# Performance work log

Measured on AMD Instinct MI355X. Metric: run time of the kernel, lower is better.

## Reference

```python
import jax, jax.numpy as jnp
from jax import lax
import numpy as np

DEPTH = 4
D_MODEL = 192
D_INNER = 384
D_STATE = 16
D_CONV = 4
DT_RANK = 12
STRIDE = 4
NUM_PATCHES = 400
L_SEQ = NUM_PATCHES + 1  # +1 cls token appended at the end
EPS = 1e-5


def _rmsnorm(x, w):
    x = x.astype(jnp.float32)
    return (x * lax.rsqrt(jnp.mean(x * x, axis=-1, keepdims=True) + EPS)) * w


def _mamba(x, in_w, cw, cb, xp_w, dtw, dtb, A_log, Dv, ow):
    # x: [B, L, D_MODEL]
    B = x.shape[0]
    xz = jnp.einsum('bld,ed->ble', x, in_w)            # [B, L, 2*D_INNER]
    u, z = jnp.split(xz, 2, axis=-1)                   # [B, L, D_INNER] each
    # causal depthwise conv over L
    u_t = jnp.transpose(u, (0, 2, 1))                  # [B, D_INNER, L]
    u_pad = jnp.pad(u_t, ((0, 0), (0, 0), (D_CONV - 1, 0)))
    conv = lax.conv_general_dilated(
        u_pad, cw[:, None, :], (1,), 'VALID',
        dimension_numbers=('NCH', 'OIH', 'NCH'),
        feature_group_count=D_INNER)                   # [B, D_INNER, L]
    u = jax.nn.silu(conv + cb[:, None])
    u = jnp.transpose(u, (0, 2, 1))                    # [B, L, D_INNER]
    xdbl = jnp.einsum('bld,ed->ble', u, xp_w)          # [B, L, 44]
    dt, Bm, Cm = jnp.split(xdbl, [DT_RANK, DT_RANK + D_STATE], axis=-1)
    dt = jax.nn.softplus(jnp.einsum('blr,dr->bld', dt, dtw) + dtb)  # [B, L, D_INNER]
    A = -jnp.exp(A_log)                                # [D_INNER, D_STATE]
    dA = jnp.exp(dt[..., None] * A)                    # [B, L, D_INNER, D_STATE]
    dBu = dt[..., None] * Bm[:, :, None, :] * u[..., None]
    h0 = jnp.zeros((B, D_INNER, D_STATE), dtype=dA.dtype)

    def step(h, inp):
        dA_t, dBu_t = inp
        h = dA_t * h + dBu_t
        return h, h

    _, hs = lax.scan(step, h0, (jnp.swapaxes(dA, 0, 1), jnp.swapaxes(dBu, 0, 1)))
    hs = jnp.swapaxes(hs, 0, 1)                        # [B, L, D_INNER, D_STATE]
    y = jnp.einsum('bldn,bln->bld', hs, Cm) + u * Dv
    y = y * jax.nn.silu(z)
    return jnp.einsum('bld,ed->ble', y, ow)            # [B, L, D_MODEL]


def _forward(imgs, patch_w, patch_b, pos_embed, cls_token, norm_w, in_proj_w,
             conv_w, conv_b, xproj_w, dt_w, dt_b, A_log, D_param, out_w,
             normf_w, head_w, head_b):
    B = imgs.shape[0]
    # StrideEmbed: non-overlapping strides of 4 bytes -> linear to embed_dim
    x = imgs.reshape(B, NUM_PATCHES, STRIDE) @ patch_w + patch_b  # [B, 400, 192]
    x = x + pos_embed[:, :-1, :]
    cls = cls_token + pos_embed[:, -1:, :]             # [1, 1, 192]
    x = jnp.concatenate([x, jnp.broadcast_to(cls, (B, 1, D_MODEL))], axis=1)
    hidden = x
    residual = None
    for i in range(DEPTH):
        residual = hidden if residual is None else hidden + residual  # fp32 residual stream
        h = _rmsnorm(residual, norm_w[i])
        hidden = _mamba(h, in_proj_w[i], conv_w[i], conv_b[i], xproj_w[i],
                        dt_w[i], dt_b[i], A_log[i], D_param[i], out_w[i])
    x = _rmsnorm(hidden + residual, normf_w)
    cls_out = x[:, -1, :]                              # [B, 192]
    logits = cls_out @ head_w.T + head_b               # [B, 1000]
    return logits


def setup_inputs() -> dict:
    key = jax.random.key(0)
    ks = jax.random.split(key, 16)
    B = 32
    rn = lambda k, s, sc: jax.random.normal(k, s, dtype=jnp.float32) * sc
    A_log = jnp.broadcast_to(jnp.log(jnp.arange(1.0, D_STATE + 1.0, dtype=jnp.float32)),
                             (DEPTH, D_INNER, D_STATE))
    return {
        'imgs': rn(ks[0], (B, 1, 40, 40), 1.0),
        'patch_w': rn(ks[1], (STRIDE, D_MODEL), 0.1),
        'patch_b': jnp.zeros((D_MODEL,), jnp.float32),
        'pos_embed': rn(ks[2], (1, L_SEQ, D_MODEL), 0.02),
        'cls_token': rn(ks[3], (1, 1, D_MODEL), 0.02),
        'norm_w': jnp.ones((DEPTH, D_MODEL), jnp.float32),
        'in_proj_w': rn(ks[4], (DEPTH, 2 * D_INNER, D_MODEL), 0.05),
        'conv_w': rn(ks[5], (DEPTH, D_INNER, D_CONV), 0.3),
        'conv_b': jnp.zeros((DEPTH, D_INNER), jnp.float32),
        'xproj_w': rn(ks[6], (DEPTH, DT_RANK + 2 * D_STATE, D_INNER), 0.05),
        'dt_w': rn(ks[7], (DEPTH, D_INNER, DT_RANK), 0.1),
        'dt_b': rn(ks[8], (DEPTH, D_INNER), 0.5) - 4.0,
        'A_log': A_log,
        'D_param': jnp.ones((DEPTH, D_INNER), jnp.float32),
        'out_w': rn(ks[9], (DEPTH, D_MODEL, D_INNER), 0.05),
        'normf_w': jnp.ones((D_MODEL,), jnp.float32),
        'head_w': rn(ks[10], (1000, D_MODEL), 0.05),
        'head_b': jnp.zeros((1000,), jnp.float32),
    }


def reference(imgs, patch_w, patch_b, pos_embed, cls_token, norm_w, in_proj_w,
              conv_w, conv_b, xproj_w, dt_w, dt_b, A_log, D_param, out_w,
              normf_w, head_w, head_b):
    return _forward(imgs, patch_w, patch_b, pos_embed, cls_token, norm_w,
                    in_proj_w, conv_w, conv_b, xproj_w, dt_w, dt_b, A_log,
                    D_param, out_w, normf_w, head_w, head_b)
```

## Files before the change

### kernel.cpp

```cpp
#include <hip/hip_runtime.h>
#include <hip/hip_bf16.h>

#define B_SZ 32
#define LSEQ 401
#define NT (B_SZ * LSEQ)
#define DM 192
#define DI 384
#define DS 16
#define EPSF 1e-5f
#define NCH 16

typedef __attribute__((ext_vector_type(8))) short short8;
typedef __attribute__((ext_vector_type(4))) float f32x4;
typedef __hip_bfloat16 bf16;

#define OFF_IMGS    0
#define OFF_PATCHW  51200
#define OFF_PATCHB  51968
#define OFF_POS     52160
#define OFF_CLS     129152
#define OFF_NORMW   129344
#define OFF_INW     130112
#define OFF_CONVW   719936
#define OFF_CONVB   726080
#define OFF_XPROJW  727616
#define OFF_DTW     795200
#define OFF_DTB     813632
#define OFF_ALOG    815168
#define OFF_DP      839744
#define OFF_OUTW    841280
#define OFF_NORMF   1136192
#define OFF_HEADW   1136384
#define OFF_HEADB   1328384
#define OFF_TOTAL   1329384

#define WB_INW   0
#define WB_XPJ   589824
#define WB_OUT   688128
#define WB_DTW   983040
#define WB_TOTAL 1032192

__device__ __forceinline__ int chunk_s(int c) { return c == 0 ? 0 : 25 * c + 1; }
__device__ __forceinline__ int chunk_e(int c) { return 25 * c + 26; }

__device__ __forceinline__ float ldsrc(const void* p, int off, int isbf) {
  return isbf ? __bfloat162float(((const bf16*)p)[off]) : ((const float*)p)[off];
}
__device__ __forceinline__ float fast_silu(float z) {
  return z * __builtin_amdgcn_rcpf(1.f + __expf(-z));
}
__device__ __forceinline__ float fast_softplus(float x) {
  float e = __expf(x);
  return (x > 15.f) ? x : __logf(1.f + e);
}
__device__ __forceinline__ float bfbits(unsigned short u) {
  return __uint_as_float(((unsigned int)u) << 16);
}

#define DPP_ADD(x, ctrl) \
  x += __int_as_float(__builtin_amdgcn_update_dpp(0, __float_as_int(x), ctrl, 0xF, 0xF, true))
__device__ __forceinline__ float row_sum16(float x) {
  DPP_ADD(x, 0xB1);
  DPP_ADD(x, 0x4E);
  DPP_ADD(x, 0x124);
  DPP_ADD(x, 0x128);
  return x;
}

struct P18 { const void* p[18]; };

__global__ __launch_bounds__(256) void k_convwb(P18 t, float* __restrict__ fin,
                                                bf16* __restrict__ wb) {
  static const int st[19] = {OFF_IMGS, OFF_PATCHW, OFF_PATCHB, OFF_POS, OFF_CLS,
                             OFF_NORMW, OFF_INW, OFF_CONVW, OFF_CONVB, OFF_XPROJW,
                             OFF_DTW, OFF_DTB, OFF_ALOG, OFF_DP, OFF_OUTW,
                             OFF_NORMF, OFF_HEADW, OFF_HEADB, OFF_TOTAL};
  int isbf = (((const unsigned short*)t.p[5])[0] == 0x3F80) ? 1 : 0;
  int idx = blockIdx.x * 256 + threadIdx.x;
  if (idx < OFF_TOTAL) {
    int lo = 0;
#pragma unroll
    for (int i = 1; i < 18; ++i) if (idx >= st[i]) lo = i;
    fin[idx] = ldsrc(t.p[lo], idx - st[lo], isbf);
  } else if (idx < OFF_TOTAL + WB_TOTAL) {
    int j = idx - OFF_TOTAL;
    float v;
    if (j < WB_XPJ) {
      v = ldsrc(t.p[6], j, isbf);
    } else if (j < WB_OUT) {
      int i2 = j - WB_XPJ;
      int l = i2 / (64 * 384);
      int r = (i2 / 384) & 63;
      int k = i2 % 384;
      v = (r < 44) ? ldsrc(t.p[9], l * 44 * 384 + r * 384 + k, isbf) : 0.f;
    } else if (j < WB_DTW) {
      v = ldsrc(t.p[14], j - WB_OUT, isbf);
    } else {
      int i2 = j - WB_DTW;
      int l = i2 / (384 * 32);
      int r = i2 % (384 * 32);
      int d = r >> 5;
      int k = r & 31;
      v = (k < 12) ? ldsrc(t.p[10], l * 4608 + d * 12 + k, isbf) : 0.f;
    }
    wb[j] = __float2bfloat16(v);
  }
}

__device__ __forceinline__ void inproj32(const bf16 (*shb)[200],
                                         const bf16* __restrict__ Win,
                                         bf16* __restrict__ xb,
                                         bf16* __restrict__ zb,
                                         int row0, int tid) {
  int lane = tid & 63, wave = tid >> 6;
  int q = lane >> 4, mlo = lane & 15;
  short8 afrA[6], afrB[6];
#pragma unroll
  for (int kk = 0; kk < 6; ++kk) {
    afrA[kk] = *(const short8*)&shb[mlo][kk * 32 + q * 8];
    afrB[kk] = *(const short8*)&shb[16 + mlo][kk * 32 + q * 8];
  }
  const bf16* wbase = Win + (size_t)(wave * 96 + mlo) * DM + q * 8;
#pragma unroll
  for (int jh = 0; jh < 2; ++jh) {
    short8 Bb[18];
#pragma unroll
    for (int j = 0; j < 3; ++j)
#pragma unroll
      for (int kk = 0; kk < 6; ++kk)
        Bb[j * 6 + kk] = *(const short8*)(wbase + (size_t)(jh * 3 + j) * 16 * DM + kk * 32);
#pragma unroll
    for (int j = 0; j < 3; ++j) {
      f32x4 aA = {}, aB = {};
#pragma unroll
      for (int kk = 0; kk < 6; ++kk) {
        aA = __builtin_amdgcn_mfma_f32_16x16x32_bf16(afrA[kk], Bb[j * 6 + kk], aA, 0, 0, 0);
        aB = __builtin_amdgcn_mfma_f32_16x16x32_bf16(afrB[kk], Bb[j * 6 + kk], aB, 0, 0, 0);
      }
      int n = wave * 96 + (jh * 3 + j) * 16 + mlo;
      if (n < DI) {
#pragma unroll
        for (int i = 0; i < 4; ++i) {
          xb[(size_t)(row0 + q * 4 + i) * DI + n] = __float2bfloat16(aA[i]);
          xb[(size_t)(row0 + 16 + q * 4 + i) * DI + n] = __float2bfloat16(aB[i]);
        }
      } else {
        int nz = n - DI;
#pragma unroll
        for (int i = 0; i < 4; ++i) {
          zb[(size_t)(row0 + q * 4 + i) * DI + nz] = __float2bfloat16(aA[i]);
          zb[(size_t)(row0 + 16 + q * 4 + i) * DI + nz] = __float2bfloat16(aB[i]);
        }
      }
    }
  }
}

__global__ __launch_bounds__(512)
__attribute__((amdgpu_waves_per_eu(2, 2)))
void k_embedin(const float* __restrict__ fin,
               float* __restrict__ residual,
               const bf16* __restrict__ Win,
               bf16* __restrict__ xb,
               bf16* __restrict__ zb) {
  __shared__ bf16 shb[32][200];
  const float* imgs = fin + OFF_IMGS;
  const float* pw   = fin + OFF_PATCHW;
  const float* pb   = fin + OFF_PATCHB;
  const float* pos  = fin + OFF_POS;
  const float* cls  = fin + OFF_CLS;
  const float* nw0  = fin + OFF_NORMW;
  int tid = threadIdx.x;
  int row0 = blockIdx.x * 32;
  {
    int row = tid >> 4, g = tid & 15;
    int t = row0 + row;
    int b = t / LSEQ, l = t % LSEQ;
    float im[4];
    if (l < 400) {
#pragma unroll
      for (int s = 0; s < 4; ++s) im[s] = imgs[b * 1600 + l * 4 + s];
    }
    float rn[12], ss = 0.f;
#pragma unroll
    for (int k = 0; k < 12; ++k) {
      int col = g + 16 * k;
      float v;
      if (l < 400) {
        v = pb[col] + pos[l * DM + col];
#pragma unroll
        for (int s = 0; s < 4; ++s) v = fmaf(im[s], pw[s * DM + col], v);
      } else {
        v = cls[col] + pos[400 * DM + col];
      }
      residual[(size_t)t * DM + col] = v;
      rn[k] = v;
      ss = fmaf(v, v, ss);
    }
    ss = row_sum16(ss);
    float sres = rsqrtf(ss / (float)DM + EPSF);
#pragma unroll
    for (int k = 0; k < 12; ++k) {
      int col = g + 16 * k;
      shb[row][col] = __float2bfloat16(rn[k] * sres * nw0[col]);
    }
  }
  __syncthreads();
  inproj32(shb, Win, xb, zb, row0, tid);
}

__global__ __launch_bounds__(512) void k_xdt(const bf16* __restrict__ xb,
                                             const float* __restrict__ cw,
                                             const float* __restrict__ cb,
                                             const bf16* __restrict__ Wbf,
                                             float* __restrict__ xdbl,
                                             const bf16* __restrict__ dtwb,
                                             const float* __restrict__ dtb,
                                             bf16* __restrict__ ub,
                                             bf16* __restrict__ dto) {
  __shared__ bf16  sxt[19][392];
  __shared__ bf16  su[16][392];
  __shared__ float4 scw4[384];
  __shared__ float scb[384];
  __shared__ float sxp[2][16][48];
  __shared__ bf16  sxb[16][32];
  int row0 = blockIdx.x * 16;
  int tid = threadIdx.x;
  for (int i = tid; i < 19 * 48; i += 512) {
    int r = i / 48, c8 = i - r * 48;
    int t = row0 - 3 + r;
    if (t < 0) t = 0;
    *(short8*)&sxt[r][c8 * 8] = *(const short8*)(xb + (size_t)t * DI + c8 * 8);
  }
  for (int i = tid; i < 384; i += 512) {
    scw4[i] = ((const float4*)cw)[i];
    scb[i] = cb[i];
  }
  __syncthreads();
  for (int i = tid; i < 768; i += 512) {
    int tok = i / 48;
    int c8 = i - tok * 48;
    int d0 = c8 * 8;
    int t = row0 + tok;
    int l = t % LSEQ;
    float xr[4][8];
#pragma unroll
    for (int k = 0; k < 4; ++k) {
      short8 v = *(const short8*)&sxt[tok + k][d0];
      bool ok = (l - 3 + k) >= 0;
#pragma unroll
      for (int j = 0; j < 8; ++j) {
        unsigned int uu = ((unsigned int)(unsigned short)v[j]) << 16;
        xr[k][j] = ok ? __uint_as_float(uu) : 0.f;
      }
    }
    short8 uvv;
#pragma unroll
    for (int j = 0; j < 8; ++j) {
      float4 w = scw4[d0 + j];
      float a = scb[d0 + j];
      a = fmaf(xr[0][j], w.x, a);
      a = fmaf(xr[1][j], w.y, a);
      a = fmaf(xr[2][j], w.z, a);
      a = fmaf(xr[3][j], w.w, a);
      bf16 h = __float2bfloat16(fast_silu(a));
      uvv[j] = *reinterpret_cast<short*>(&h);
    }
    *(short8*)&su[tok][d0] = uvv;
    *(short8*)(ub + (size_t)t * DI + d0) = uvv;
  }
  __syncthreads();
  int lane = tid & 63;
  int wave = tid >> 6;
  int q = lane >> 4;
  int mlo = lane & 15;
  if (wave < 6) {
    int colw = (wave % 3) * 16;
    int kh = wave / 3;
    f32x4 acc = {};
    for (int k0 = 0; k0 < 192; k0 += 32) {
      short8 a = *(const short8*)&su[mlo][kh * 192 + k0 + q * 8];
      short8 b = *(const short8*)(Wbf + (size_t)(colw + mlo) * DI + kh * 192 + k0 + q * 8);
      acc = __builtin_amdgcn_mfma_f32_16x16x32_bf16(a, b, acc, 0, 0, 0);
    }
#pragma unroll
    for (int i = 0; i < 4; ++i) sxp[kh][q * 4 + i][colw + mlo] = acc[i];
  }
  __syncthreads();
  for (int i = tid; i < 16 * 44; i += 512) {
    int r = i / 44, c = i - r * 44;
    xdbl[(size_t)(row0 + r) * 44 + c] = sxp[0][r][c] + sxp[1][r][c];
  }
  for (int i = tid; i < 512; i += 512) {
    int tok = i >> 5, k = i & 31;
    sxb[tok][k] = __float2bfloat16(k < 12 ? sxp[0][tok][k] + sxp[1][tok][k] : 0.f);
  }
  __syncthreads();
  short8 afrag = *(const short8*)&sxb[mlo][q * 8];
#pragma unroll
  for (int jt = 0; jt < 3; ++jt) {
    int d = (wave * 3 + jt) * 16 + mlo;
    short8 bfrag = *(const short8*)(dtwb + (size_t)d * 32 + q * 8);
    f32x4 acc = {};
    acc = __builtin_amdgcn_mfma_f32_16x16x32_bf16(afrag, bfrag, acc, 0, 0, 0);
    float dtbv = dtb[d];
#pragma unroll
    for (int i = 0; i < 4; ++i)
      dto[(size_t)(row0 + q * 4 + i) * DI + d] =
          __float2bfloat16(fast_softplus(acc[i] + dtbv));
  }
}

__global__ __launch_bounds__(384)
__attribute__((amdgpu_waves_per_eu(2, 2)))
void k_scanA(const bf16* __restrict__ ub,
             const bf16* __restrict__ dtv,
             const float* __restrict__ xdbl,
             const float* __restrict__ A_log,
             float* __restrict__ Sq,
             float* __restrict__ Hq) {
  __shared__ float sB[26][16];
  int cc = blockIdx.x, b = blockIdx.y;
  int d = threadIdx.x;
  int s = chunk_s(cc), tc = chunk_e(cc) - s;
  int base = b * LSEQ;
  for (int i = d; i < tc * 16; i += 384) {
    int t = i >> 4, col = i & 15;
    sB[t][col] = xdbl[(size_t)(base + s + t) * 44 + 12 + col];
  }
  __syncthreads();
  float A[16], h[16];
#pragma unroll
  for (int j = 0; j < 4; ++j) {
    f32x4 al = *(const f32x4*)&A_log[d * DS + j * 4];
#pragma unroll
    for (int i = 0; i < 4; ++i) { A[j * 4 + i] = -__expf(al[i]); h[j * 4 + i] = 0.f; }
  }
  float S = 0.f;
  const unsigned short* pd = (const unsigned short*)(dtv + (size_t)(base + s) * DI + d);
  const unsigned short* pu = (const unsigned short*)(ub  + (size_t)(base + s) * DI + d);
  unsigned short dN = *pd, uN = *pu;
  for (int t = 0; t < tc; ++t) {
    unsigned short dC = dN, uC = uN;
    if (t + 1 < tc) { pd += DI; pu += DI; dN = *pd; uN = *pu; }
    float dv = bfbits(dC), uv = bfbits(uC);
    float w = dv * uv;
    S += dv;
    f32x4 B0 = *(const f32x4*)&sB[t][0];
    f32x4 B1 = *(const f32x4*)&sB[t][4];
    f32x4 B2 = *(const f32x4*)&sB[t][8];
    f32x4 B3 = *(const f32x4*)&sB[t][12];
#pragma unroll
    for (int n = 0; n < 16; ++n) {
      float Bn = (n < 4) ? B0[n] : (n < 8) ? B1[n - 4] : (n < 12) ? B2[n - 8] : B3[n - 12];
      float E = __expf(dv * A[n]);
      h[n] = fmaf(E, h[n], w * Bn);
    }
  }
  size_t si = ((size_t)cc * B_SZ + b) * 384 + d;
  Sq[si] = S;
#pragma unroll
  for (int j = 0; j < 4; ++j) {
    f32x4 hv;
#pragma unroll
    for (int i = 0; i < 4; ++i) hv[i] = h[j * 4 + i];
    *(f32x4*)&Hq[si * 16 + j * 4] = hv;
  }
}

__global__ __launch_bounds__(256) void k_scanP(const float* __restrict__ A_log,
                                               const float* __restrict__ Sq,
                                               float* __restrict__ Hq) {
  int idx = blockIdx.x * 256 + threadIdx.x;
  int n = idx & 15;
  int dd = (idx >> 4) % 384;
  int b = idx / (384 * 16);
  float A = -__expf(A_log[dd * DS + n]);
  float hs = 0.f;
  for (int c = 0; c < NCH - 1; ++c) {
    size_t si = ((size_t)c * B_SZ + b) * 384 + dd;
    float P = __expf(A * Sq[si]);
    size_t hi = si * 16 + n;
    float he = Hq[hi];
    hs = fmaf(P, hs, he);
    Hq[hi] = hs;
  }
}

__global__ __launch_bounds__(384)
__attribute__((amdgpu_waves_per_eu(2, 2)))
void k_scanB(const bf16* __restrict__ zb,
             const bf16* __restrict__ ub,
             const bf16* __restrict__ dtv,
             const float* __restrict__ xdbl,
             const float* __restrict__ A_log,
             const float* __restrict__ Dp,
             const float* __restrict__ Hq,
             bf16* __restrict__ yb) {
  __shared__ float sB[26][16], sC[26][16];
  int cc = blockIdx.x, b = blockIdx.y;
  int d = threadIdx.x;
  int s = chunk_s(cc), tc = chunk_e(cc) - s;
  int base = b * LSEQ;
  for (int i = d; i < tc * 32; i += 384) {
    int t = i >> 5, col = i & 31;
    float v = xdbl[(size_t)(base + s + t) * 44 + 12 + col];
    if (col < 16) sB[t][col] = v;
    else          sC[t][col - 16] = v;
  }
  __syncthreads();
  float A[16], h[16];
#pragma unroll
  for (int j = 0; j < 4; ++j) {
    f32x4 al = *(const f32x4*)&A_log[d * DS + j * 4];
#pragma unroll
    for (int i = 0; i < 4; ++i) A[j * 4 + i] = -__expf(al[i]);
  }
  if (cc == 0) {
#pragma unroll
    for (int n = 0; n < 16; ++n) h[n] = 0.f;
  } else {
    size_t hi = (((size_t)(cc - 1) * B_SZ + b) * 384 + d) * 16;
#pragma unroll
    for (int j = 0; j < 4; ++j) {
      f32x4 hv = *(const f32x4*)&Hq[hi + j * 4];
#pragma unroll
      for (int i = 0; i < 4; ++i) h[j * 4 + i] = hv[i];
    }
  }
  float Dv = Dp[d];
  const unsigned short* pd = (const unsigned short*)(dtv + (size_t)(base + s) * DI + d);
  const unsigned short* pu = (const unsigned short*)(ub  + (size_t)(base + s) * DI + d);
  const unsigned short* pz = (const unsigned short*)(zb  + (size_t)(base + s) * DI + d);
  bf16* py = yb + (size_t)(base + s) * DI + d;
  unsigned short dN = *pd, uN = *pu, zN = *pz;
  for (int t = 0; t < tc; ++t) {
    unsigned short dC = dN, uC = uN, zC = zN;
    if (t + 1 < tc) { pd += DI; pu += DI; pz += DI; dN = *pd; uN = *pu; zN = *pz; }
    float dv = bfbits(dC), uv = bfbits(uC), zv = bfbits(zC);
    float w = dv * uv;
    f32x4 B0 = *(const f32x4*)&sB[t][0];
    f32x4 B1 = *(const f32x4*)&sB[t][4];
    f32x4 B2 = *(const f32x4*)&sB[t][8];
    f32x4 B3 = *(const f32x4*)&sB[t][12];
    f32x4 C0 = *(const f32x4*)&sC[t][0];
    f32x4 C1 = *(const f32x4*)&sC[t][4];
    f32x4 C2 = *(const f32x4*)&sC[t][8];
    f32x4 C3 = *(const f32x4*)&sC[t][12];
    float y0 = 0.f, y1 = 0.f;
#pragma unroll
    for (int n = 0; n < 16; ++n) {
      float Bn = (n < 4) ? B0[n] : (n < 8) ? B1[n - 4] : (n < 12) ? B2[n - 8] : B3[n - 12];
      float Cn = (n < 4) ? C0[n] : (n < 8) ? C1[n - 4] : (n < 12) ? C2[n - 8] : C3[n - 12];
      float E = __expf(dv * A[n]);
      h[n] = fmaf(E, h[n], w * Bn);
      if (n & 1) y1 = fmaf(h[n], Cn, y1);
      else       y0 = fmaf(h[n], Cn, y0);
    }
    float yv = (y0 + y1 + uv * Dv) * fast_silu(zv);
    *py = __float2bfloat16(yv);
    py += DI;
  }
}

__global__ __launch_bounds__(512)
__attribute__((amdgpu_waves_per_eu(2, 2)))
void k_outin(const bf16* __restrict__ yb,
             const bf16* __restrict__ Wout,
             float* __restrict__ residual,
             const float* __restrict__ nw,
             const bf16* __restrict__ Win,
             bf16* __restrict__ xb,
             bf16* __restrict__ zb) {
  __shared__ bf16  syt[32][392];
  __shared__ float sCt[2][32][200];
  __shared__ bf16  shb[32][200];
  int tid = threadIdx.x;
  int lane = tid & 63;
  int wave = tid >> 6;
  int row0 = blockIdx.x * 32;
  int q = lane >> 4;
  int mlo = lane & 15;
  {
    int i0 = tid, i1 = tid + 512, i2 = tid + 1024;
    const bf16* src = yb + (size_t)row0 * DI;
    short8 v0 = *(const short8*)(src + (i0 / 48) * DI + (i0 % 48) * 8);
    short8 v1 = *(const short8*)(src + (i1 / 48) * DI + (i1 % 48) * 8);
    short8 v2 = *(const short8*)(src + (i2 / 48) * DI + (i2 % 48) * 8);
    *(short8*)&syt[i0 / 48][(i0 % 48) * 8] = v0;
    *(short8*)&syt[i1 / 48][(i1 % 48) * 8] = v1;
    *(short8*)&syt[i2 / 48][(i2 % 48) * 8] = v2;
  }
  __syncthreads();
  {
    int colw = (wave & 3) * 48;
    int kh = wave >> 2;
    const bf16* brow = Wout + (size_t)(colw + mlo) * DI + kh * 192 + q * 8;
    short8 Bf[18];
#pragma unroll
    for (int j = 0; j < 3; ++j)
#pragma unroll
      for (int k2 = 0; k2 < 6; ++k2)
        Bf[j * 6 + k2] = *(const short8*)(brow + (size_t)j * 16 * DI + k2 * 32);
    short8 afA[6], afB[6];
#pragma unroll
    for (int k2 = 0; k2 < 6; ++k2) {
      afA[k2] = *(const short8*)&syt[mlo][kh * 192 + k2 * 32 + q * 8];
      afB[k2] = *(const short8*)&syt[16 + mlo][kh * 192 + k2 * 32 + q * 8];
    }
    f32x4 acc[2][3] = {};
#pragma unroll
    for (int k2 = 0; k2 < 6; ++k2) {
#pragma unroll
      for (int j = 0; j < 3; ++j) {
        acc[0][j] = __builtin_amdgcn_mfma_f32_16x16x32_bf16(afA[k2], Bf[j * 6 + k2], acc[0][j], 0, 0, 0);
        acc[1][j] = __builtin_amdgcn_mfma_f32_16x16x32_bf16(afB[k2], Bf[j * 6 + k2], acc[1][j], 0, 0, 0);
      }
    }
#pragma unroll
    for (int rg = 0; rg < 2; ++rg)
#pragma unroll
      for (int j = 0; j < 3; ++j)
#pragma unroll
        for (int i = 0; i < 4; ++i)
          sCt[kh][rg * 16 + q * 4 + i][colw + j * 16 + mlo] = acc[rg][j][i];
  }
  __syncthreads();
  {
    int row = tid >> 4, g = tid & 15;
    int t = row0 + row;
    float* rp = residual + (size_t)t * DM + g * 12;
    float4 r4[3];
#pragma unroll
    for (int j = 0; j < 3; ++j) r4[j] = *(const float4*)(rp + j * 4);
    float rn[12], ss = 0.f;
#pragma unroll
    for (int k = 0; k < 12; ++k) {
      int col = g * 12 + k;
      float x = sCt[0][row][col] + sCt[1][row][col] + ((const float*)r4)[k];
      rn[k] = x;
      ss = fmaf(x, x, ss);
    }
    ss = row_sum16(ss);
    float sres = rsqrtf(ss / (float)DM + EPSF);
#pragma unroll
    for (int j = 0; j < 3; ++j) {
      float4 w4;
      w4.x = rn[j * 4 + 0]; w4.y = rn[j * 4 + 1];
      w4.z = rn[j * 4 + 2]; w4.w = rn[j * 4 + 3];
      *(float4*)(rp + j * 4) = w4;
    }
#pragma unroll
    for (int k = 0; k < 12; ++k) {
      int col = g * 12 + k;
      shb[row][col] = __float2bfloat16(rn[k] * sres * nw[col]);
    }
  }
  __syncthreads();
  inproj32(shb, Win, xb, zb, row0, tid);
}

__global__ __launch_bounds__(256) void k_lastout(const bf16* __restrict__ yb,
                                                 const bf16* __restrict__ Wout,
                                                 const float* __restrict__ resIn,
                                                 float* __restrict__ clsbuf) {
  __shared__ float sCt[16][200];
  int tid = threadIdx.x;
  int lane = tid & 63;
  int wave = tid >> 6;
  int b0 = blockIdx.x * 16;
  int q = lane >> 4;
  int mlo = lane & 15;
  int colw = wave * 48;
  f32x4 acc[3] = {};
  const bf16* arow = yb + ((size_t)(b0 + mlo) * LSEQ + 400) * DI + q * 8;
  for (int k0 = 0; k0 < DI; k0 += 32) {
    short8 a = *(const short8*)(arow + k0);
#pragma unroll
    for (int j = 0; j < 3; ++j) {
      short8 b = *(const short8*)(Wout + (size_t)(colw + j * 16 + mlo) * DI + k0 + q * 8);
      acc[j] = __builtin_amdgcn_mfma_f32_16x16x32_bf16(a, b, acc[j], 0, 0, 0);
    }
  }
#pragma unroll
  for (int j = 0; j < 3; ++j)
#pragma unroll
    for (int i = 0; i < 4; ++i) sCt[q * 4 + i][colw + j * 16 + mlo] = acc[j][i];
  __syncthreads();
  int row = tid >> 4, g = tid & 15;
  int bb = b0 + row;
#pragma unroll
  for (int k = 0; k < 12; ++k) {
    int col = g + 16 * k;
    clsbuf[(size_t)bb * DM + col] =
        sCt[row][col] + resIn[((size_t)bb * LSEQ + 400) * DM + col];
  }
}

__global__ __launch_bounds__(256) void k_final(const float* __restrict__ clsbuf,
                                               const float* __restrict__ fin,
                                               const void* __restrict__ nw_raw,
                                               void* __restrict__ out) {
  const float* normf  = fin + OFF_NORMF;
  const float* head_w = fin + OFF_HEADW;
  const float* head_b = fin + OFF_HEADB;
  __shared__ float clsv[DM];
  __shared__ float partial[4];
  __shared__ float sres;
  int b = blockIdx.x;
  float r = 0.f;
  if (threadIdx.x < DM) r = clsbuf[(size_t)b * DM + threadIdx.x];
  float ss = r * r;
#pragma unroll
  for (int m = 32; m >= 1; m >>= 1) ss += __shfl_xor(ss, m, 64);
  if ((threadIdx.x & 63) == 0) partial[threadIdx.x >> 6] = ss;
  __syncthreads();
  if (threadIdx.x == 0)
    sres = rsqrtf((partial[0] + partial[1] + partial[2] + partial[3]) / (float)DM + EPSF);
  __syncthreads();
  if (threadIdx.x < DM) clsv[threadIdx.x] = r * sres * normf[threadIdx.x];
  __syncthreads();
  int isbf = (((const unsigned short*)nw_raw)[0] == 0x3F80) ? 1 : 0;
  for (int e = threadIdx.x; e < 1000; e += 256) {
    float acc = head_b[e];
    for (int k = 0; k < DM; ++k) acc = fmaf(clsv[k], head_w[e * DM + k], acc);
    if (isbf) ((bf16*)out)[b * 1000 + e] = __float2bfloat16(acc);
    else      ((float*)out)[b * 1000 + e] = acc;
  }
}

extern "C" void kernel_launch(void* const* d_in, const int* in_sizes, int n_in,
                              void* d_out, int out_size, void* d_ws, size_t ws_size,
                              hipStream_t stream) {
  char* base = (char*)d_ws;
  size_t off = 0;
  auto alloc = [&](size_t bytes) { char* p = base + off; off = (off + bytes + 255) & ~(size_t)255; return p; };
  float* fin      = (float*)alloc((size_t)OFF_TOTAL * 4);
  bf16*  wb       = (bf16*)alloc((size_t)WB_TOTAL * 2);
  float* residual = (float*)alloc((size_t)NT * DM * 4);
  bf16*  xb       = (bf16*)alloc((size_t)NT * DI * 2);
  bf16*  zb       = (bf16*)alloc((size_t)NT * DI * 2);
  bf16*  ub       = (bf16*)alloc((size_t)NT * DI * 2);
  float* xdbl     = (float*)alloc((size_t)NT * 44 * 4);
  bf16*  dtb16    = (bf16*)alloc((size_t)NT * DI * 2);
  float* Sq       = (float*)alloc((size_t)(NCH - 1) * B_SZ * 384 * 4);
  float* Hq       = (float*)alloc((size_t)(NCH - 1) * B_SZ * 384 * 16 * 4);
  float* clsbuf   = (float*)alloc((size_t)B_SZ * DM * 4);
  bf16*  yb       = ub;

  P18 t;
  for (int i = 0; i < 18; ++i) t.p[i] = d_in[i];
  k_convwb<<<(OFF_TOTAL + WB_TOTAL + 255) / 256, 256, 0, stream>>>(t, fin, wb);

  k_embedin<<<NT / 32, 512, 0, stream>>>(fin, residual, wb + WB_INW, xb, zb);

  for (int layer = 0; layer < 4; ++layer) {
    const float* dtb = fin + OFF_DTB + layer * DI;
    const float* alog = fin + OFF_ALOG + layer * DI * DS;

    k_xdt<<<NT / 16, 512, 0, stream>>>(xb, fin + OFF_CONVW + layer * DI * 4,
                                       fin + OFF_CONVB + layer * DI,
                                       wb + WB_XPJ + layer * 64 * DI, xdbl,
                                       wb + WB_DTW + layer * 384 * 32, dtb, ub, dtb16);

    k_scanA<<<dim3(NCH - 1, B_SZ), 384, 0, stream>>>(ub, dtb16, xdbl, alog, Sq, Hq);
    k_scanP<<<(B_SZ * 384 * 16) / 256, 256, 0, stream>>>(alog, Sq, Hq);
    k_scanB<<<dim3(NCH, B_SZ), 384, 0, stream>>>(zb, ub, dtb16, xdbl, alog,
                                                 fin + OFF_DP + layer * DI, Hq, yb);

    if (layer < 3) {
      k_outin<<<NT / 32, 512, 0, stream>>>(yb, wb + WB_OUT + layer * DM * DI, residual,
                                           fin + OFF_NORMW + (layer + 1) * DM,
                                           wb + WB_INW + (layer + 1) * 768 * DM, xb, zb);
    } else {
      k_lastout<<<2, 256, 0, stream>>>(yb, wb + WB_OUT + 3 * DM * DI, residual, clsbuf);
    }
  }
  k_final<<<B_SZ, 256, 0, stream>>>(clsbuf, fin, d_in[5], d_out);
}
```

Before: 594.9 us.

## Drop scan prefix kernel and halve block size of embed/outin kernels

```diff
diff --git a/kernel.cpp b/kernel.cpp
--- a/kernel.cpp
+++ b/kernel.cpp
@@ -107,11 +107,11 @@
   }
 }
 
-__device__ __forceinline__ void inproj32(const bf16 (*shb)[200],
-                                         const bf16* __restrict__ Win,
-                                         bf16* __restrict__ xb,
-                                         bf16* __restrict__ zb,
-                                         int row0, int tid) {
+__device__ __forceinline__ void inproj_4w(const bf16 (*shb)[200],
+                                          const bf16* __restrict__ Win,
+                                          bf16* __restrict__ xb,
+                                          bf16* __restrict__ zb,
+                                          int row0, int tid) {
   int lane = tid & 63, wave = tid >> 6;
   int q = lane >> 4, mlo = lane & 15;
   short8 afrA[6], afrB[6];
@@ -120,9 +120,11 @@
     afrA[kk] = *(const short8*)&shb[mlo][kk * 32 + q * 8];
     afrB[kk] = *(const short8*)&shb[16 + mlo][kk * 32 + q * 8];
   }
-  const bf16* wbase = Win + (size_t)(wave * 96 + mlo) * DM + q * 8;
-#pragma unroll
-  for (int jh = 0; jh < 2; ++jh) {
+  const bf16* wbase = Win + (size_t)(wave * 192 + mlo) * DM + q * 8;
+  bf16* dst = (wave < 2) ? xb : zb;
+  int ncol0 = (wave < 2) ? wave * 192 : (wave - 2) * 192;
+#pragma unroll
+  for (int jh = 0; jh < 4; ++jh) {
     short8 Bb[18];
 #pragma unroll
     for (int j = 0; j < 3; ++j)
@@ -137,26 +139,17 @@
         aA = __builtin_amdgcn_mfma_f32_16x16x32_bf16(afrA[kk], Bb[j * 6 + kk], aA, 0, 0, 0);
         aB = __builtin_amdgcn_mfma_f32_16x16x32_bf16(afrB[kk], Bb[j * 6 + kk], aB, 0, 0, 0);
       }
-      int n = wave * 96 + (jh * 3 + j) * 16 + mlo;
-      if (n < DI) {
-#pragma unroll
-        for (int i = 0; i < 4; ++i) {
-          xb[(size_t)(row0 + q * 4 + i) * DI + n] = __float2bfloat16(aA[i]);
-          xb[(size_t)(row0 + 16 + q * 4 + i) * DI + n] = __float2bfloat16(aB[i]);
-        }
-      } else {
-        int nz = n - DI;
-#pragma unroll
-        for (int i = 0; i < 4; ++i) {
-          zb[(size_t)(row0 + q * 4 + i) * DI + nz] = __float2bfloat16(aA[i]);
-          zb[(size_t)(row0 + 16 + q * 4 + i) * DI + nz] = __float2bfloat16(aB[i]);
-        }
+      int n = ncol0 + (jh * 3 + j) * 16 + mlo;
+#pragma unroll
+      for (int i = 0; i < 4; ++i) {
+        dst[(size_t)(row0 + q * 4 + i) * DI + n] = __float2bfloat16(aA[i]);
+        dst[(size_t)(row0 + 16 + q * 4 + i) * DI + n] = __float2bfloat16(aB[i]);
       }
     }
   }
 }
 
-__global__ __launch_bounds__(512)
+__global__ __launch_bounds__(256)
 __attribute__((amdgpu_waves_per_eu(2, 2)))
 void k_embedin(const float* __restrict__ fin,
                float* __restrict__ residual,
@@ -172,8 +165,9 @@
   const float* nw0  = fin + OFF_NORMW;
   int tid = threadIdx.x;
   int row0 = blockIdx.x * 32;
-  {
-    int row = tid >> 4, g = tid & 15;
+#pragma unroll
+  for (int rr = 0; rr < 2; ++rr) {
+    int row = rr * 16 + (tid >> 4), g = tid & 15;
     int t = row0 + row;
     int b = t / LSEQ, l = t % LSEQ;
     float im[4];
@@ -206,7 +200,7 @@
     }
   }
   __syncthreads();
-  inproj32(shb, Win, xb, zb, row0, tid);
+  inproj_4w(shb, Win, xb, zb, row0, tid);
 }
 
 __global__ __launch_bounds__(512) void k_xdt(const bf16* __restrict__ xb,
@@ -317,7 +311,7 @@
              const bf16* __restrict__ dtv,
              const float* __restrict__ xdbl,
              const float* __restrict__ A_log,
-             float* __restrict__ Sq,
+             float* __restrict__ Pq,
              float* __restrict__ Hq) {
   __shared__ float sB[26][16];
   int cc = blockIdx.x, b = blockIdx.y;
@@ -357,33 +351,17 @@
       h[n] = fmaf(E, h[n], w * Bn);
     }
   }
-  size_t si = ((size_t)cc * B_SZ + b) * 384 + d;
-  Sq[si] = S;
+  size_t si = (((size_t)cc * B_SZ + b) * 384 + d) * 16;
 #pragma unroll
   for (int j = 0; j < 4; ++j) {
-    f32x4 hv;
-#pragma unroll
-    for (int i = 0; i < 4; ++i) hv[i] = h[j * 4 + i];
-    *(f32x4*)&Hq[si * 16 + j * 4] = hv;
-  }
-}
-
-__global__ __launch_bounds__(256) void k_scanP(const float* __restrict__ A_log,
-                                               const float* __restrict__ Sq,
-                                               float* __restrict__ Hq) {
-  int idx = blockIdx.x * 256 + threadIdx.x;
-  int n = idx & 15;
-  int dd = (idx >> 4) % 384;
-  int b = idx / (384 * 16);
-  float A = -__expf(A_log[dd * DS + n]);
-  float hs = 0.f;
-  for (int c = 0; c < NCH - 1; ++c) {
-    size_t si = ((size_t)c * B_SZ + b) * 384 + dd;
-    float P = __expf(A * Sq[si]);
-    size_t hi = si * 16 + n;
-    float he = Hq[hi];
-    hs = fmaf(P, hs, he);
-    Hq[hi] = hs;
+    f32x4 hv, pv;
+#pragma unroll
+    for (int i = 0; i < 4; ++i) {
+      hv[i] = h[j * 4 + i];
+      pv[i] = __expf(A[j * 4 + i] * S);
+    }
+    *(f32x4*)&Hq[si + j * 4] = hv;
+    *(f32x4*)&Pq[si + j * 4] = pv;
   }
 }
 
@@ -395,6 +373,7 @@
              const float* __restrict__ xdbl,
              const float* __restrict__ A_log,
              const float* __restrict__ Dp,
+             const float* __restrict__ Pq,
              const float* __restrict__ Hq,
              bf16* __restrict__ yb) {
   __shared__ float sB[26][16], sC[26][16];
@@ -414,18 +393,17 @@
   for (int j = 0; j < 4; ++j) {
     f32x4 al = *(const f32x4*)&A_log[d * DS + j * 4];
 #pragma unroll
-    for (int i = 0; i < 4; ++i) A[j * 4 + i] = -__expf(al[i]);
-  }
-  if (cc == 0) {
-#pragma unroll
-    for (int n = 0; n < 16; ++n) h[n] = 0.f;
-  } else {
-    size_t hi = (((size_t)(cc - 1) * B_SZ + b) * 384 + d) * 16;
+    for (int i = 0; i < 4; ++i) { A[j * 4 + i] = -__expf(al[i]); h[j * 4 + i] = 0.f; }
+  }
+  for (int c = 0; c < cc; ++c) {
+    size_t si = (((size_t)c * B_SZ + b) * 384 + d) * 16;
 #pragma unroll
     for (int j = 0; j < 4; ++j) {
-      f32x4 hv = *(const f32x4*)&Hq[hi + j * 4];
-#pragma unroll
-      for (int i = 0; i < 4; ++i) h[j * 4 + i] = hv[i];
+      f32x4 pv = *(const f32x4*)&Pq[si + j * 4];
+      f32x4 hv = *(const f32x4*)&Hq[si + j * 4];
+#pragma unroll
+      for (int i = 0; i < 4; ++i)
+        h[j * 4 + i] = fmaf(pv[i], h[j * 4 + i], hv[i]);
     }
   }
   float Dv = Dp[d];
@@ -463,7 +441,7 @@
   }
 }
 
-__global__ __launch_bounds__(512)
+__global__ __launch_bounds__(256)
 __attribute__((amdgpu_waves_per_eu(2, 2)))
 void k_outin(const bf16* __restrict__ yb,
              const bf16* __restrict__ Wout,
@@ -473,7 +451,7 @@
              bf16* __restrict__ xb,
              bf16* __restrict__ zb) {
   __shared__ bf16  syt[32][392];
-  __shared__ float sCt[2][32][200];
+  __shared__ float sCt[32][200];
   __shared__ bf16  shb[32][200];
   int tid = threadIdx.x;
   int lane = tid & 63;
@@ -482,40 +460,46 @@
   int q = lane >> 4;
   int mlo = lane & 15;
   {
-    int i0 = tid, i1 = tid + 512, i2 = tid + 1024;
     const bf16* src = yb + (size_t)row0 * DI;
-    short8 v0 = *(const short8*)(src + (i0 / 48) * DI + (i0 % 48) * 8);
-    short8 v1 = *(const short8*)(src + (i1 / 48) * DI + (i1 % 48) * 8);
-    short8 v2 = *(const short8*)(src + (i2 / 48) * DI + (i2 % 48) * 8);
-    *(short8*)&syt[i0 / 48][(i0 % 48) * 8] = v0;
-    *(short8*)&syt[i1 / 48][(i1 % 48) * 8] = v1;
-    *(short8*)&syt[i2 / 48][(i2 % 48) * 8] = v2;
+    short8 v[6];
+#pragma unroll
+    for (int j = 0; j < 6; ++j) {
+      int i = tid + j * 256;
+      v[j] = *(const short8*)(src + (i / 48) * DI + (i % 48) * 8);
+    }
+#pragma unroll
+    for (int j = 0; j < 6; ++j) {
+      int i = tid + j * 256;
+      *(short8*)&syt[i / 48][(i % 48) * 8] = v[j];
+    }
   }
   __syncthreads();
   {
-    int colw = (wave & 3) * 48;
-    int kh = wave >> 2;
-    const bf16* brow = Wout + (size_t)(colw + mlo) * DI + kh * 192 + q * 8;
-    short8 Bf[18];
-#pragma unroll
-    for (int j = 0; j < 3; ++j)
-#pragma unroll
-      for (int k2 = 0; k2 < 6; ++k2)
-        Bf[j * 6 + k2] = *(const short8*)(brow + (size_t)j * 16 * DI + k2 * 32);
-    short8 afA[6], afB[6];
-#pragma unroll
-    for (int k2 = 0; k2 < 6; ++k2) {
-      afA[k2] = *(const short8*)&syt[mlo][kh * 192 + k2 * 32 + q * 8];
-      afB[k2] = *(const short8*)&syt[16 + mlo][kh * 192 + k2 * 32 + q * 8];
-    }
+    int colw = wave * 48;
     f32x4 acc[2][3] = {};
 #pragma unroll
-    for (int k2 = 0; k2 < 6; ++k2) {
-#pragma unroll
-      for (int j = 0; j < 3; ++j) {
-        acc[0][j] = __builtin_amdgcn_mfma_f32_16x16x32_bf16(afA[k2], Bf[j * 6 + k2], acc[0][j], 0, 0, 0);
-        acc[1][j] = __builtin_amdgcn_mfma_f32_16x16x32_bf16(afB[k2], Bf[j * 6 + k2], acc[1][j], 0, 0, 0);
+    for (int kh = 0; kh < 2; ++kh) {
+      const bf16* brow = Wout + (size_t)(colw + mlo) * DI + kh * 192 + q * 8;
+      short8 Bf[18];
+#pragma unroll
+      for (int j = 0; j < 3; ++j)
+#pragma unroll
+        for (int k2 = 0; k2 < 6; ++k2)
+          Bf[j * 6 + k2] = *(const short8*)(brow + (size_t)j * 16 * DI + k2 * 32);
+      short8 afA[6], afB[6];
+#pragma unroll
+      for (int k2 = 0; k2 < 6; ++k2) {
+        afA[k2] = *(const short8*)&syt[mlo][kh * 192 + k2 * 32 + q * 8];
+        afB[k2] = *(const short8*)&syt[16 + mlo][kh * 192 + k2 * 32 + q * 8];
       }
+#pragma unroll
+      for (int k2 = 0; k2 < 6; ++k2) {
+#pragma unroll
+        for (int j = 0; j < 3; ++j) {
+          acc[0][j] = __builtin_amdgcn_mfma_f32_16x16x32_bf16(afA[k2], Bf[j * 6 + k2], acc[0][j], 0, 0, 0);
+          acc[1][j] = __builtin_amdgcn_mfma_f32_16x16x32_bf16(afB[k2], Bf[j * 6 + k2], acc[1][j], 0, 0, 0);
+        }
+      }
     }
 #pragma unroll
     for (int rg = 0; rg < 2; ++rg)
@@ -523,11 +507,12 @@
       for (int j = 0; j < 3; ++j)
 #pragma unroll
         for (int i = 0; i < 4; ++i)
-          sCt[kh][rg * 16 + q * 4 + i][colw + j * 16 + mlo] = acc[rg][j][i];
-  }
-  __syncthreads();
-  {
-    int row = tid >> 4, g = tid & 15;
+          sCt[rg * 16 + q * 4 + i][colw + j * 16 + mlo] = acc[rg][j][i];
+  }
+  __syncthreads();
+#pragma unroll
+  for (int rr = 0; rr < 2; ++rr) {
+    int row = rr * 16 + (tid >> 4), g = tid & 15;
     int t = row0 + row;
     float* rp = residual + (size_t)t * DM + g * 12;
     float4 r4[3];
@@ -537,7 +522,7 @@
 #pragma unroll
     for (int k = 0; k < 12; ++k) {
       int col = g * 12 + k;
-      float x = sCt[0][row][col] + sCt[1][row][col] + ((const float*)r4)[k];
+      float x = sCt[row][col] + ((const float*)r4)[k];
       rn[k] = x;
       ss = fmaf(x, x, ss);
     }
@@ -557,7 +542,7 @@
     }
   }
   __syncthreads();
-  inproj32(shb, Win, xb, zb, row0, tid);
+  inproj_4w(shb, Win, xb, zb, row0, tid);
 }
 
 __global__ __launch_bounds__(256) void k_lastout(const bf16* __restrict__ yb,
@@ -643,7 +628,7 @@
   bf16*  ub       = (bf16*)alloc((size_t)NT * DI * 2);
   float* xdbl     = (float*)alloc((size_t)NT * 44 * 4);
   bf16*  dtb16    = (bf16*)alloc((size_t)NT * DI * 2);
-  float* Sq       = (float*)alloc((size_t)(NCH - 1) * B_SZ * 384 * 4);
+  float* Pq       = (float*)alloc((size_t)(NCH - 1) * B_SZ * 384 * 16 * 4);
   float* Hq       = (float*)alloc((size_t)(NCH - 1) * B_SZ * 384 * 16 * 4);
   float* clsbuf   = (float*)alloc((size_t)B_SZ * DM * 4);
   bf16*  yb       = ub;
@@ -652,7 +637,7 @@
   for (int i = 0; i < 18; ++i) t.p[i] = d_in[i];
   k_convwb<<<(OFF_TOTAL + WB_TOTAL + 255) / 256, 256, 0, stream>>>(t, fin, wb);
 
-  k_embedin<<<NT / 32, 512, 0, stream>>>(fin, residual, wb + WB_INW, xb, zb);
+  k_embedin<<<NT / 32, 256, 0, stream>>>(fin, residual, wb + WB_INW, xb, zb);
 
   for (int layer = 0; layer < 4; ++layer) {
     const float* dtb = fin + OFF_DTB + layer * DI;
@@ -663,13 +648,12 @@
                                        wb + WB_XPJ + layer * 64 * DI, xdbl,
                                        wb + WB_DTW + layer * 384 * 32, dtb, ub, dtb16);
 
-    k_scanA<<<dim3(NCH - 1, B_SZ), 384, 0, stream>>>(ub, dtb16, xdbl, alog, Sq, Hq);
-    k_scanP<<<(B_SZ * 384 * 16) / 256, 256, 0, stream>>>(alog, Sq, Hq);
+    k_scanA<<<dim3(NCH - 1, B_SZ), 384, 0, stream>>>(ub, dtb16, xdbl, alog, Pq, Hq);
     k_scanB<<<dim3(NCH, B_SZ), 384, 0, stream>>>(zb, ub, dtb16, xdbl, alog,
-                                                 fin + OFF_DP + layer * DI, Hq, yb);
+                                                 fin + OFF_DP + layer * DI, Pq, Hq, yb);
 
     if (layer < 3) {
-      k_outin<<<NT / 32, 512, 0, stream>>>(yb, wb + WB_OUT + layer * DM * DI, residual,
+      k_outin<<<NT / 32, 256, 0, stream>>>(yb, wb + WB_OUT + layer * DM * DI, residual,
                                            fin + OFF_NORMW + (layer + 1) * DM,
                                            wb + WB_INW + (layer + 1) * 768 * DM, xb, zb);
     } else {
```

After: 662.1 us. +11.3%, slower.
